# Optimization experiments

Measured on AMD Instinct MI355X. Metric: run time of the kernel, lower is better.

The kernel has to match this reference:

```python
import jax, jax.numpy as jnp
import numpy as np

P = 4096          # n_patch (64x64 grid)
S = 64            # grid side
L = 9             # 9-neighbor window
E = 34            # attention embed dim (32 hidden + 2 coords)
H = 32            # hidden size
N_OBS = 10
N_PRED = 50


def _neighbor_flat_idx():
    idx = np.arange(P)
    r, c = idx // S, idx % S
    off = np.array([[-1,-1],[-1,0],[-1,1],[0,-1],[0,0],[0,1],[1,-1],[1,0],[1,1]])
    nr = (r[:, None] + off[:, 0]).reshape(S, S, L)
    nc = (c[:, None] + off[:, 1]).reshape(S, S, L)
    # boundary shift (as in the torch module)
    nr[0] += 1; nr[-1] -= 1
    nc[:, 0] += 1; nc[:, -1] -= 1
    return jnp.asarray((nr * S + nc).reshape(P, L))  # [P, 9] into patch dim


def _patch_label(B):
    coords = jnp.arange(S, dtype=jnp.float32) / S
    pl = jnp.stack(jnp.meshgrid(coords, coords, indexing='ij'), -1).reshape(P, 2)
    return jnp.broadcast_to(pl[:, None, :], (P, B, 2))  # [P, B, 2]


def setup_inputs() -> dict:
    key = jax.random.key(0)
    ks = jax.random.split(key, 8)
    s = 0.1
    return {
        'x': jax.random.normal(ks[0], (N_OBS, 2 * P, H), jnp.float32),
        'W_x2h': jax.random.normal(ks[1], (H, H), jnp.float32) * s,
        'b_x2h': jnp.zeros((H,), jnp.float32),
        'W_h2h': jax.random.normal(ks[2], (H, H), jnp.float32) * s,
        'b_h2h': jnp.zeros((H,), jnp.float32),
        'W_fc2': jax.random.normal(ks[3], (H, H), jnp.float32) * s,
        'b_fc2': jnp.zeros((H,), jnp.float32),
        'ln_g': jnp.ones((H,), jnp.float32),
        'ln_b': jnp.zeros((H,), jnp.float32),
        'W_fcsa': jax.random.normal(ks[4], (H, E), jnp.float32) * s,
        'b_fcsa': jnp.zeros((H,), jnp.float32),
        'W_in': jax.random.normal(ks[5], (3 * E, E), jnp.float32) * s,
        'b_in': jnp.zeros((3 * E,), jnp.float32),
        'W_out': jax.random.normal(ks[6], (E, E), jnp.float32) * s,
        'b_out': jnp.zeros((E,), jnp.float32),
    }


def reference(x, W_x2h, b_x2h, W_h2h, b_h2h, W_fc2, b_fc2, ln_g, ln_b,
              W_fcsa, b_fcsa, W_in, b_in, W_out, b_out):
    B = x.shape[1] // P
    N = B * P
    nbr = _neighbor_flat_idx()
    pl = _patch_label(B)

    def layernorm(y):
        mu = jnp.mean(y, -1, keepdims=True)
        var = jnp.mean((y - mu) ** 2, -1, keepdims=True)
        return (y - mu) * jax.lax.rsqrt(var + 1e-5) * ln_g + ln_b

    def mha(xa):  # [L, N, E] self-attention, 1 head
        qkv = xa @ W_in.T + b_in
        q, k, v = jnp.split(qkv, 3, axis=-1)
        scores = jnp.einsum('lne,mne->nlm', q, k) / jnp.sqrt(jnp.float32(E))
        w = jax.nn.softmax(scores, axis=-1)
        o = jnp.einsum('nlm,mne->lne', w, v)
        return o @ W_out.T + b_out

    def step(h, inp):
        h = jnp.tanh(inp @ W_x2h.T + b_x2h + h @ W_h2h.T + b_h2h)  # [N, H]
        hb = jnp.transpose(h.reshape(B, P, H), (1, 0, 2))          # [P, B, H]
        qin = jnp.concatenate([hb, pl], -1)                        # [P, B, E]
        nq = qin[nbr]                                              # [P, 9, B, E]
        xa = jnp.transpose(nq, (1, 2, 0, 3)).reshape(L, N, E)      # [9, N, E]
        ao = mha(xa)[4]                                            # center, [N, E]
        h = h + ao @ W_fcsa.T + b_fcsa
        pred = layernorm(h @ W_fc2.T + b_fc2)
        return h, pred

    h0 = jnp.zeros((N, H), x.dtype)
    h, preds_obs = jax.lax.scan(step, h0, x)                       # [10, N, H]

    def step_pred(carry, _):
        h, p = carry
        h, pnew = step(h, p)
        return (h, pnew), pnew

    _, preds_fut = jax.lax.scan(step_pred, (h, preds_obs[-1]), None,
                                length=N_PRED - 1)                 # [49, N, H]
    return jnp.concatenate([preds_obs, preds_fut], 0)              # [59, N, H]
```

## Files before the change

kernel.cpp:

```cpp
#include <hip/hip_runtime.h>

#define NROWS 8192
#define RPB   32
#define TPB   1024
#define NBLK  256

#define OFF_W1   0
#define OFF_W2   1024
#define OFF_WIN  2048
#define OFF_WFC2 5516
#define OFF_M    6540
#define OFF_B12  7628
#define OFF_BIN  7660
#define OFF_B2   7762
#define OFF_BFC2 7794
#define OFF_LNG  7826
#define OFF_LNB  7858
#define OFF_QKV0 8192
#define QKVN     (NROWS*102)
#define OFF_QKV1 (OFF_QKV0 + QKVN)
#define OFF_HNEW (OFF_QKV1 + QKVN)

__global__ __launch_bounds__(256) void setup_kernel(
    const float* __restrict__ W_x2h, const float* __restrict__ b_x2h,
    const float* __restrict__ W_h2h, const float* __restrict__ b_h2h,
    const float* __restrict__ W_fc2, const float* __restrict__ b_fc2,
    const float* __restrict__ ln_g,  const float* __restrict__ ln_b,
    const float* __restrict__ W_fcsa,const float* __restrict__ b_fcsa,
    const float* __restrict__ W_in,  const float* __restrict__ b_in,
    const float* __restrict__ W_out, const float* __restrict__ b_out,
    float* __restrict__ ws)
{
  int t = blockIdx.x*blockDim.x + threadIdx.x;
  int stride = gridDim.x*blockDim.x;
  for (int i=t;i<1024;i+=stride) ws[OFF_W1+i]   = W_x2h[i];
  for (int i=t;i<1024;i+=stride) ws[OFF_W2+i]   = W_h2h[i];
  for (int i=t;i<3468;i+=stride) ws[OFF_WIN+i]  = W_in[i];
  for (int i=t;i<1024;i+=stride) ws[OFF_WFC2+i] = W_fc2[i];
  for (int i=t;i<32;i+=stride)   ws[OFF_B12+i]  = b_x2h[i] + b_h2h[i];
  for (int i=t;i<102;i+=stride)  ws[OFF_BIN+i]  = b_in[i];
  for (int i=t;i<32;i+=stride)   ws[OFF_BFC2+i] = b_fc2[i];
  for (int i=t;i<32;i+=stride)   ws[OFF_LNG+i]  = ln_g[i];
  for (int i=t;i<32;i+=stride)   ws[OFF_LNB+i]  = ln_b[i];
  for (int idx=t; idx<1088; idx+=stride) {
    int j = idx/34, f = idx - j*34;
    float acc = 0.f;
    for (int e=0;e<34;++e)
      acc += W_fcsa[j*34+e] * W_out[e*34+f];
    ws[OFF_M+idx] = acc;
  }
  for (int j=t;j<32;j+=stride){
    float acc = b_fcsa[j];
    for (int e=0;e<34;++e) acc += W_fcsa[j*34+e] * b_out[e];
    ws[OFF_B2+j] = acc;
  }
}

__global__ __launch_bounds__(TPB) void step_kernel(
    const float* __restrict__ ws,
    const float* __restrict__ qkvR,
    float* __restrict__ qkvW,
    float* __restrict__ hnewG,
    const float* __restrict__ x,
    float* __restrict__ out,
    int stepB, int stepA)
{
  __shared__ float sW1[32][32], sW2[32][32], sWfc2[32][32];
  __shared__ float sM[32][36];
  __shared__ float sWin[102][36];
  __shared__ float sB12[32], sBin[102], sB2[32], sBfc2[32], sLng[32], sLnb[32];
  __shared__ float sS[RPB][13];
  __shared__ float sO[RPB][35];
  __shared__ float sHp[RPB][33];
  __shared__ float sG[RPB][33];
  __shared__ float sPred[RPB][33];
  __shared__ float sHn[RPB][33];
  __shared__ float sX[RPB][33];

  const int tid  = threadIdx.x;
  const int lr2  = tid & 31;
  const int slot = tid >> 5;
  const int base = blockIdx.x * RPB;
  const int r2   = base + lr2;
  const int b    = base >> 12;
  const int p    = base & 4095;
  const int gr   = p >> 6;
  const int gc0  = p & 63;
  const int c    = gc0 + lr2;
  const int br   = (gr < 1) ? 1 : ((gr > 62) ? 62 : gr);
  const int bc   = (c  < 1) ? 1 : ((c  > 62) ? 62 : c);

  {
    sW1  [tid>>5][tid&31] = ws[OFF_W1  +tid];
    sW2  [tid>>5][tid&31] = ws[OFF_W2  +tid];
    sWfc2[tid>>5][tid&31] = ws[OFF_WFC2+tid];
    for (int idx=tid; idx<1088; idx+=TPB){ int j=idx/34, e=idx-j*34; sM[j][e]=ws[OFF_M+idx]; }
    for (int idx=tid; idx<3468; idx+=TPB){ int e=idx/34, f=idx-e*34; sWin[e][f]=ws[OFF_WIN+idx]; }
    if (tid < 102)                    sBin [tid]     = ws[OFF_BIN +tid];
    else if (tid>=128 && tid<160)     sB12 [tid-128] = ws[OFF_B12 +tid-128];
    else if (tid>=160 && tid<192)     sB2  [tid-160] = ws[OFF_B2  +tid-160];
    else if (tid>=192 && tid<224)     sBfc2[tid-192] = ws[OFF_BFC2+tid-192];
    else if (tid>=224 && tid<256)     sLng [tid-224] = ws[OFF_LNG +tid-224];
    else if (tid>=256 && tid<288)     sLnb [tid-256] = ws[OFF_LNB +tid-256];
  }
  if (stepA >= 0 && stepA < 10) {
    size_t xbase = ((size_t)stepA*NROWS + base)*32;
    sX[tid>>5][tid&31] = x[xbase + tid];
  }
  if (stepB >= 0) {
    if (slot >= 16) {
      const int j0 = (slot-16)*2;
      sHp[lr2][j0]   = hnewG[(size_t)j0    *NROWS + r2];
      sHp[lr2][j0+1] = hnewG[(size_t)(j0+1)*NROWS + r2];
    } else if (slot < 9) {
      const int m  = slot;
      const int dr = m/3 - 1, dc = m - (m/3)*3 - 1;
      const int qrow = (b<<12) + (br<<6) + bc;
      const int nr_  = (b<<12) + ((br+dr)<<6) + (bc+dc);
      float acc = 0.f;
      #pragma unroll
      for (int e=0;e<34;++e)
        acc += qkvR[(size_t)e*NROWS + qrow] * qkvR[(size_t)(34+e)*NROWS + nr_];
      sS[lr2][m] = acc * 0.1714985851425088f;
    }
  } else {
    sHp[lr2][slot] = 0.f;
  }
  __syncthreads();

  if (stepB >= 0) {
    {
      float sc[9]; float mx = -1e30f;
      #pragma unroll
      for (int m=0;m<9;++m){ sc[m]=sS[lr2][m]; mx=fmaxf(mx,sc[m]); }
      float sum=0.f;
      #pragma unroll
      for (int m=0;m<9;++m){ sc[m]=__expf(sc[m]-mx); sum+=sc[m]; }
      float inv = 1.f/sum;
      float o0=0.f, o1=0.f;
      const bool e2ok = (slot < 2);
      #pragma unroll
      for (int m=0;m<9;++m){
        int dr = m/3 - 1, dc = m - (m/3)*3 - 1;
        int nr_ = (b<<12) + ((br+dr)<<6) + (bc+dc);
        float wm = sc[m]*inv;
        o0 += wm * qkvR[(size_t)(68+slot)*NROWS + nr_];
        if (e2ok) o1 += wm * qkvR[(size_t)(100+slot)*NROWS + nr_];
      }
      sO[lr2][slot] = o0;
      if (e2ok) sO[lr2][32+slot] = o1;
    }
    __syncthreads();
    {
      float a = sB2[slot];
      #pragma unroll
      for (int e=0;e<34;++e) a += sO[lr2][e] * sM[slot][e];
      sHp[lr2][slot] += a;
    }
    __syncthreads();
    {
      float g = sBfc2[slot];
      #pragma unroll
      for (int i=0;i<32;++i) g += sHp[lr2][i] * sWfc2[slot][i];
      sG[lr2][slot] = g;
    }
    __syncthreads();
    {
      float mu=0.f;
      #pragma unroll
      for (int i=0;i<32;++i) mu += sG[lr2][i];
      mu *= 0.03125f;
      float var=0.f;
      #pragma unroll
      for (int i=0;i<32;++i){ float d=sG[lr2][i]-mu; var += d*d; }
      var *= 0.03125f;
      float rs = rsqrtf(var + 1e-5f);
      sPred[lr2][slot] = (sG[lr2][slot]-mu)*rs*sLng[slot] + sLnb[slot];
    }
    __syncthreads();
    {
      size_t obase = ((size_t)stepB*NROWS + base)*32;
      out[obase + tid] = sPred[tid>>5][tid&31];
    }
  } else {
    __syncthreads(); __syncthreads(); __syncthreads(); __syncthreads();
  }

  if (stepA >= 0) {
    float a = sB12[slot];
    if (stepA < 10) {
      #pragma unroll
      for (int i=0;i<32;++i)
        a += sX[lr2][i]*sW1[slot][i] + sHp[lr2][i]*sW2[slot][i];
    } else {
      #pragma unroll
      for (int i=0;i<32;++i)
        a += sPred[lr2][i]*sW1[slot][i] + sHp[lr2][i]*sW2[slot][i];
    }
    {
      float t0 = tanhf(a);
      sHn[lr2][slot] = t0;
      hnewG[(size_t)slot*NROWS + r2] = t0;
    }
    __syncthreads();
    float hn[32];
    #pragma unroll
    for (int f=0;f<32;++f) hn[f]=sHn[lr2][f];
    const float pl0 = gr*0.015625f, pl1 = c*0.015625f;
    #pragma unroll
    for (int k=0;k<4;++k){
      int e = slot + 32*k;
      if (e < 102) {
        float acc = sBin[e];
        #pragma unroll
        for (int f=0;f<32;++f) acc += hn[f]*sWin[e][f];
        acc += pl0*sWin[e][32] + pl1*sWin[e][33];
        qkvW[(size_t)e*NROWS + r2] = acc;
      }
    }
  }
}

extern "C" void kernel_launch(void* const* d_in, const int* in_sizes, int n_in,
                              void* d_out, int out_size, void* d_ws, size_t ws_size,
                              hipStream_t stream) {
  const float* x     = (const float*)d_in[0];
  const float* W_x2h = (const float*)d_in[1];
  const float* b_x2h = (const float*)d_in[2];
  const float* W_h2h = (const float*)d_in[3];
  const float* b_h2h = (const float*)d_in[4];
  const float* W_fc2 = (const float*)d_in[5];
  const float* b_fc2 = (const float*)d_in[6];
  const float* ln_g  = (const float*)d_in[7];
  const float* ln_b  = (const float*)d_in[8];
  const float* W_fcsa= (const float*)d_in[9];
  const float* b_fcsa= (const float*)d_in[10];
  const float* W_in  = (const float*)d_in[11];
  const float* b_in  = (const float*)d_in[12];
  const float* W_out = (const float*)d_in[13];
  const float* b_out = (const float*)d_in[14];
  float* ws = (float*)d_ws;
  float* out = (float*)d_out;

  setup_kernel<<<8, 256, 0, stream>>>(W_x2h,b_x2h,W_h2h,b_h2h,W_fc2,b_fc2,ln_g,ln_b,
                                      W_fcsa,b_fcsa,W_in,b_in,W_out,b_out, ws);
  for (int i=0;i<60;++i){
    int stepB = i-1;
    int stepA = (i<=58)? i : -1;
    const float* qR = ws + OFF_QKV0 + (size_t)((i+1)&1)*QKVN;
    float*       qW = ws + OFF_QKV0 + (size_t)(i&1)*QKVN;
    step_kernel<<<NBLK, TPB, 0, stream>>>(ws, qR, qW, ws+OFF_HNEW, x, out, stepB, stepA);
  }
}
```

Baseline: 962.6 us.

## Remap post-attention stages to wave-local rows with shuffle layernorm and fewer barriers

The attention-projection, fc2 and layernorm stages now give each 64-lane wave two complete rows of 32 features. Block-wide __syncthreads between these stages become a wave-local LDS wait, and the layernorm mean and variance are reduced with xor shuffles instead of every thread re-reading 32 values from shared memory. The weight tiles in shared memory are padded (33/35 columns) so per-lane row indexing avoids bank conflicts. Output is written directly from registers. The price is an extra shared buffer for the previous hidden state and a dependence on wavefront size 64.

```diff
diff --git a/kernel.cpp b/kernel.cpp
--- a/kernel.cpp
+++ b/kernel.cpp
@@ -4,6 +4,11 @@
 #define RPB   32
 #define TPB   1024
 #define NBLK  256
+#define SCALE 0.1714985851425088f
+#define INV64 0.015625f
+
+#define WFENCE() do { asm volatile("s_waitcnt lgkmcnt(0)" ::: "memory"); \
+                      __builtin_amdgcn_sched_barrier(0); } while (0)
 
 #define OFF_W1   0
 #define OFF_W2   1024
@@ -65,14 +70,14 @@
     float* __restrict__ out,
     int stepB, int stepA)
 {
-  __shared__ float sW1[32][32], sW2[32][32], sWfc2[32][32];
-  __shared__ float sM[32][36];
+  __shared__ float sW1[32][33], sW2[32][33], sWfc2[32][33];
+  __shared__ float sM[32][35];
   __shared__ float sWin[102][36];
   __shared__ float sB12[32], sBin[102], sB2[32], sBfc2[32], sLng[32], sLnb[32];
   __shared__ float sS[RPB][13];
   __shared__ float sO[RPB][35];
+  __shared__ float sHprev[RPB][33];
   __shared__ float sHp[RPB][33];
-  __shared__ float sG[RPB][33];
   __shared__ float sPred[RPB][33];
   __shared__ float sHn[RPB][33];
   __shared__ float sX[RPB][33];
@@ -80,6 +85,9 @@
   const int tid  = threadIdx.x;
   const int lr2  = tid & 31;
   const int slot = tid >> 5;
+  const int l    = tid & 63;
+  const int j2   = l & 31;
+  const int rowg = ((tid >> 6) << 1) + (l >> 5);
   const int base = blockIdx.x * RPB;
   const int r2   = base + lr2;
   const int b    = base >> 12;
@@ -110,8 +118,8 @@
   if (stepB >= 0) {
     if (slot >= 16) {
       const int j0 = (slot-16)*2;
-      sHp[lr2][j0]   = hnewG[(size_t)j0    *NROWS + r2];
-      sHp[lr2][j0+1] = hnewG[(size_t)(j0+1)*NROWS + r2];
+      sHprev[lr2][j0]   = hnewG[(size_t)j0    *NROWS + r2];
+      sHprev[lr2][j0+1] = hnewG[(size_t)(j0+1)*NROWS + r2];
     } else if (slot < 9) {
       const int m  = slot;
       const int dr = m/3 - 1, dc = m - (m/3)*3 - 1;
@@ -121,7 +129,7 @@
       #pragma unroll
       for (int e=0;e<34;++e)
         acc += qkvR[(size_t)e*NROWS + qrow] * qkvR[(size_t)(34+e)*NROWS + nr_];
-      sS[lr2][m] = acc * 0.1714985851425088f;
+      sS[lr2][m] = acc * SCALE;
     }
   } else {
     sHp[lr2][slot] = 0.f;
@@ -151,53 +159,45 @@
       if (e2ok) sO[lr2][32+slot] = o1;
     }
     __syncthreads();
+
     {
-      float a = sB2[slot];
-      #pragma unroll
-      for (int e=0;e<34;++e) a += sO[lr2][e] * sM[slot][e];
-      sHp[lr2][slot] += a;
-    }
-    __syncthreads();
-    {
-      float g = sBfc2[slot];
-      #pragma unroll
-      for (int i=0;i<32;++i) g += sHp[lr2][i] * sWfc2[slot][i];
-      sG[lr2][slot] = g;
-    }
-    __syncthreads();
-    {
-      float mu=0.f;
-      #pragma unroll
-      for (int i=0;i<32;++i) mu += sG[lr2][i];
+      float hp = sHprev[rowg][j2] + sB2[j2];
+      #pragma unroll
+      for (int e=0;e<34;++e) hp += sO[rowg][e] * sM[j2][e];
+      sHp[rowg][j2] = hp;
+      WFENCE();
+      float g = sBfc2[j2];
+      #pragma unroll
+      for (int i=0;i<32;++i) g += sHp[rowg][i] * sWfc2[j2][i];
+      float mu = g;
+      #pragma unroll
+      for (int k=1;k<32;k<<=1) mu += __shfl_xor(mu, k, 64);
       mu *= 0.03125f;
-      float var=0.f;
-      #pragma unroll
-      for (int i=0;i<32;++i){ float d=sG[lr2][i]-mu; var += d*d; }
+      float d = g - mu;
+      float var = d*d;
+      #pragma unroll
+      for (int k=1;k<32;k<<=1) var += __shfl_xor(var, k, 64);
       var *= 0.03125f;
       float rs = rsqrtf(var + 1e-5f);
-      sPred[lr2][slot] = (sG[lr2][slot]-mu)*rs*sLng[slot] + sLnb[slot];
+      float pred = d*rs*sLng[j2] + sLnb[j2];
+      sPred[rowg][j2] = pred;
+      out[((size_t)stepB*NROWS + base + rowg)*32 + j2] = pred;
     }
     __syncthreads();
+  }
+
+  if (stepA >= 0) {
     {
-      size_t obase = ((size_t)stepB*NROWS + base)*32;
-      out[obase + tid] = sPred[tid>>5][tid&31];
-    }
-  } else {
-    __syncthreads(); __syncthreads(); __syncthreads(); __syncthreads();
-  }
-
-  if (stepA >= 0) {
-    float a = sB12[slot];
-    if (stepA < 10) {
-      #pragma unroll
-      for (int i=0;i<32;++i)
-        a += sX[lr2][i]*sW1[slot][i] + sHp[lr2][i]*sW2[slot][i];
-    } else {
-      #pragma unroll
-      for (int i=0;i<32;++i)
-        a += sPred[lr2][i]*sW1[slot][i] + sHp[lr2][i]*sW2[slot][i];
-    }
-    {
+      float a = sB12[slot];
+      if (stepA < 10) {
+        #pragma unroll
+        for (int i=0;i<32;++i)
+          a += sX[lr2][i]*sW1[slot][i] + sHp[lr2][i]*sW2[slot][i];
+      } else {
+        #pragma unroll
+        for (int i=0;i<32;++i)
+          a += sPred[lr2][i]*sW1[slot][i] + sHp[lr2][i]*sW2[slot][i];
+      }
       float t0 = tanhf(a);
       sHn[lr2][slot] = t0;
       hnewG[(size_t)slot*NROWS + r2] = t0;
@@ -206,7 +206,7 @@
     float hn[32];
     #pragma unroll
     for (int f=0;f<32;++f) hn[f]=sHn[lr2][f];
-    const float pl0 = gr*0.015625f, pl1 = c*0.015625f;
+    const float pl0 = gr*INV64, pl1 = c*INV64;
     #pragma unroll
     for (int k=0;k<4;++k){
       int e = slot + 32*k;
```

Result: slower. 998.5 us (+3.7%).
